# Performance work log

Hardware: AMD Instinct MI355X
Metric: run time of the kernel (lower is better)

Reference implementation:

```python
import jax, jax.numpy as jnp
import numpy as np

EPS = 1e-08
GUMBEL_TEMP = 1.0
TOPK = 5


def setup_inputs() -> dict:
    key = jax.random.key(0)
    k1, k2, k3, k4, k5, k6 = jax.random.split(key, 6)
    return {
        "h": jax.random.normal(k1, (64, 16), dtype=jnp.float32),
        "input": jax.random.normal(k2, (64, 16), dtype=jnp.float32),
        "w_p": jax.random.normal(k3, (16, 16), dtype=jnp.float32),
        "bias": jax.random.normal(k4, (64, 16), dtype=jnp.float32),
        "U1": jax.random.uniform(k5, (64, 4, 4), dtype=jnp.float32),
        "U2": jax.random.uniform(k6, (64, 4, 4), dtype=jnp.float32),
    }


def reference(h, input, w_p, bias, U1, U2):
    B = input.shape[0]  # 64 (hardcoded in the original module)
    h = h.reshape(B, 16)

    # Conditional range-remap when |h| exceeds 100 (data-dependent -> jnp.where)
    h_min, h_max = jnp.min(h), jnp.max(h)
    out_of_range = (h_max > 100.0) | (h_min < -100.0)
    mapped = jnp.clip((h - h_min) / (h_max - h_min) * 0.6 - 0.3, -0.3, 0.3)
    h = jnp.where(out_of_range, mapped, h)

    # small matmul + bias -> logits, reshaped to (64, 4, 4)
    mask = (h @ w_p + bias).reshape(64, 4, 4)

    # Gumbel noise difference
    g1 = -jnp.log(-jnp.log(U1 + EPS) + EPS)
    g2 = -jnp.log(-jnp.log(U2 + EPS) + EPS)
    soft = jax.nn.sigmoid((mask + g1 - g2) / GUMBEL_TEMP)

    # batched per-row top-k (k=5) over the flattened 4x4 grid
    flat = soft.reshape(64, 16)
    topv, _ = jax.lax.top_k(flat, TOPK)
    fifth = topv[:, TOPK - 1].reshape(64, 1, 1)

    # straight-through hard mask
    hard_bin = (soft >= fifth).astype(soft.dtype)
    hard = jax.lax.stop_gradient(hard_bin - soft) + soft
    return hard
```

## Files before the change

kernel.cpp:

```cpp
#include <hip/hip_runtime.h>
#include <math.h>

#define G_EPS 1e-8f

__global__ __launch_bounds__(1024) void GumbelLinear_kernel(
    const float* __restrict__ h_in,
    const float* __restrict__ w_p,
    const float* __restrict__ bias,
    const float* __restrict__ U1,
    const float* __restrict__ U2,
    float* __restrict__ out)
{
    __shared__ float h_s[64][16];
    __shared__ float w_s[16][16];
    __shared__ float s_s[64][16];
    __shared__ float wmin_s[16];
    __shared__ float wmax_s[16];
    __shared__ float gmm[2];

    const int tid = threadIdx.x;
    const int b   = tid >> 4;
    const int j   = tid & 15;

    float hv = h_in[tid];
    if (tid < 256) w_s[tid >> 4][tid & 15] = w_p[tid];

    float mn = hv, mx = hv;
    #pragma unroll
    for (int off = 32; off > 0; off >>= 1) {
        mn = fminf(mn, __shfl_down(mn, off));
        mx = fmaxf(mx, __shfl_down(mx, off));
    }
    const int lane = tid & 63;
    const int wid  = tid >> 6;
    if (lane == 0) { wmin_s[wid] = mn; wmax_s[wid] = mx; }
    __syncthreads();
    if (tid == 0) {
        float m0 = wmin_s[0], m1 = wmax_s[0];
        #pragma unroll
        for (int i = 1; i < 16; ++i) {
            m0 = fminf(m0, wmin_s[i]);
            m1 = fmaxf(m1, wmax_s[i]);
        }
        gmm[0] = m0; gmm[1] = m1;
    }
    __syncthreads();
    const float gmin = gmm[0], gmax = gmm[1];

    if (gmax > 100.0f || gmin < -100.0f) {
        float m = (hv - gmin) / (gmax - gmin) * 0.6f - 0.3f;
        hv = fminf(fmaxf(m, -0.3f), 0.3f);
    }
    h_s[b][j] = hv;
    __syncthreads();

    float acc = bias[tid];
    #pragma unroll
    for (int k = 0; k < 16; ++k) acc += h_s[b][k] * w_s[k][j];

    const float u1 = U1[tid], u2 = U2[tid];
    const float g1 = -logf(-logf(u1 + G_EPS) + G_EPS);
    const float g2 = -logf(-logf(u2 + G_EPS) + G_EPS);
    const float x  = acc + g1 - g2;
    const float soft = 1.0f / (1.0f + expf(-x));

    s_s[b][j] = soft;
    __syncthreads();

    int cnt = 0;
    #pragma unroll
    for (int k = 0; k < 16; ++k) cnt += (s_s[b][k] > soft) ? 1 : 0;

    const float hb = (cnt <= 4) ? 1.0f : 0.0f;
    out[tid] = (hb - soft) + soft;
}

extern "C" void kernel_launch(void* const* d_in, const int* in_sizes, int n_in,
                              void* d_out, int out_size, void* d_ws, size_t ws_size,
                              hipStream_t stream) {
    const float* h    = (const float*)d_in[0];
    const float* w_p  = (const float*)d_in[2];
    const float* bias = (const float*)d_in[3];
    const float* U1   = (const float*)d_in[4];
    const float* U2   = (const float*)d_in[5];
    float* out = (float*)d_out;

    GumbelLinear_kernel<<<1, 1024, 0, stream>>>(h, w_p, bias, U1, U2, out);
}
```

Measured before the change: 9.676 us.

## Restructure kernel to 256 threads with float4 work and shuffle-based row exchange

Each thread now handles four consecutive elements loaded as float4, so a 16-wide row spans four lanes. The row matmul and the top-k rank counting exchange values through xor shuffles instead of shared-memory staging, which removes two block barriers and the serial reduction step. The sigmoid is dropped and ranking is done on the pre-sigmoid logits, which is valid because sigmoid is monotonic. The output is written as exact 0/1 values rather than the (hb - soft) + soft straight-through form, which may differ from the reference in the last bit.

After: 16.31 us. 68.6% more time.

```diff
diff --git a/kernel.cpp b/kernel.cpp
--- a/kernel.cpp
+++ b/kernel.cpp
@@ -3,7 +3,7 @@
 
 #define G_EPS 1e-8f
 
-__global__ __launch_bounds__(1024) void GumbelLinear_kernel(
+__global__ __launch_bounds__(256) void GumbelLinear_kernel(
     const float* __restrict__ h_in,
     const float* __restrict__ w_p,
     const float* __restrict__ bias,
@@ -11,68 +11,89 @@
     const float* __restrict__ U2,
     float* __restrict__ out)
 {
-    __shared__ float h_s[64][16];
     __shared__ float w_s[16][16];
-    __shared__ float s_s[64][16];
-    __shared__ float wmin_s[16];
-    __shared__ float wmax_s[16];
-    __shared__ float gmm[2];
+    __shared__ float pmin[4], pmax[4];
 
-    const int tid = threadIdx.x;
-    const int b   = tid >> 4;
-    const int j   = tid & 15;
+    const int t = threadIdx.x;
+    const int q = t & 3;
 
-    float hv = h_in[tid];
-    if (tid < 256) w_s[tid >> 4][tid & 15] = w_p[tid];
+    const float4 h4  = reinterpret_cast<const float4*>(h_in)[t];
+    const float4 b4  = reinterpret_cast<const float4*>(bias)[t];
+    const float4 u14 = reinterpret_cast<const float4*>(U1)[t];
+    const float4 u24 = reinterpret_cast<const float4*>(U2)[t];
 
-    float mn = hv, mx = hv;
+    if (t < 64) {
+        reinterpret_cast<float4*>(&w_s[0][0])[t] =
+            reinterpret_cast<const float4*>(w_p)[t];
+    }
+
+    float mn = fminf(fminf(h4.x, h4.y), fminf(h4.z, h4.w));
+    float mx = fmaxf(fmaxf(h4.x, h4.y), fmaxf(h4.z, h4.w));
     #pragma unroll
-    for (int off = 32; off > 0; off >>= 1) {
-        mn = fminf(mn, __shfl_down(mn, off));
-        mx = fmaxf(mx, __shfl_down(mx, off));
+    for (int off = 1; off < 64; off <<= 1) {
+        mn = fminf(mn, __shfl_xor(mn, off));
+        mx = fmaxf(mx, __shfl_xor(mx, off));
     }
-    const int lane = tid & 63;
-    const int wid  = tid >> 6;
-    if (lane == 0) { wmin_s[wid] = mn; wmax_s[wid] = mx; }
+    if ((t & 63) == 0) { pmin[t >> 6] = mn; pmax[t >> 6] = mx; }
     __syncthreads();
-    if (tid == 0) {
-        float m0 = wmin_s[0], m1 = wmax_s[0];
-        #pragma unroll
-        for (int i = 1; i < 16; ++i) {
-            m0 = fminf(m0, wmin_s[i]);
-            m1 = fmaxf(m1, wmax_s[i]);
-        }
-        gmm[0] = m0; gmm[1] = m1;
+    const float gmin = fminf(fminf(pmin[0], pmin[1]), fminf(pmin[2], pmin[3]));
+    const float gmax = fmaxf(fmaxf(pmax[0], pmax[1]), fmaxf(pmax[2], pmax[3]));
+
+    float hx = h4.x, hy = h4.y, hz = h4.z, hw = h4.w;
+    if (gmax > 100.0f || gmin < -100.0f) {
+        const float r = gmax - gmin;
+        hx = fminf(fmaxf((hx - gmin) / r * 0.6f - 0.3f, -0.3f), 0.3f);
+        hy = fminf(fmaxf((hy - gmin) / r * 0.6f - 0.3f, -0.3f), 0.3f);
+        hz = fminf(fmaxf((hz - gmin) / r * 0.6f - 0.3f, -0.3f), 0.3f);
+        hw = fminf(fmaxf((hw - gmin) / r * 0.6f - 0.3f, -0.3f), 0.3f);
     }
-    __syncthreads();
-    const float gmin = gmm[0], gmax = gmm[1];
 
-    if (gmax > 100.0f || gmin < -100.0f) {
-        float m = (hv - gmin) / (gmax - gmin) * 0.6f - 0.3f;
-        hv = fminf(fmaxf(m, -0.3f), 0.3f);
+    float4 acc = b4;
+    const int jb = q << 2;
+    #pragma unroll
+    for (int m = 0; m < 4; ++m) {
+        const float v0 = __shfl_xor(hx, m);
+        const float v1 = __shfl_xor(hy, m);
+        const float v2 = __shfl_xor(hz, m);
+        const float v3 = __shfl_xor(hw, m);
+        const int kq = (q ^ m) << 2;
+        const float4 w0 = *reinterpret_cast<const float4*>(&w_s[kq + 0][jb]);
+        const float4 w1 = *reinterpret_cast<const float4*>(&w_s[kq + 1][jb]);
+        const float4 w2 = *reinterpret_cast<const float4*>(&w_s[kq + 2][jb]);
+        const float4 w3 = *reinterpret_cast<const float4*>(&w_s[kq + 3][jb]);
+        acc.x += v0 * w0.x + v1 * w1.x + v2 * w2.x + v3 * w3.x;
+        acc.y += v0 * w0.y + v1 * w1.y + v2 * w2.y + v3 * w3.y;
+        acc.z += v0 * w0.z + v1 * w1.z + v2 * w2.z + v3 * w3.z;
+        acc.w += v0 * w0.w + v1 * w1.w + v2 * w2.w + v3 * w3.w;
     }
-    h_s[b][j] = hv;
-    __syncthreads();
 
-    float acc = bias[tid];
+    const float xx = acc.x + logf(-logf(u24.x + G_EPS) + G_EPS) - logf(-logf(u14.x + G_EPS) + G_EPS);
+    const float xy = acc.y + logf(-logf(u24.y + G_EPS) + G_EPS) - logf(-logf(u14.y + G_EPS) + G_EPS);
+    const float xz = acc.z + logf(-logf(u24.z + G_EPS) + G_EPS) - logf(-logf(u14.z + G_EPS) + G_EPS);
+    const float xw = acc.w + logf(-logf(u24.w + G_EPS) + G_EPS) - logf(-logf(u14.w + G_EPS) + G_EPS);
+
+    int cx = (xy > xx) + (xz > xx) + (xw > xx);
+    int cy = (xx > xy) + (xz > xy) + (xw > xy);
+    int cz = (xx > xz) + (xy > xz) + (xw > xz);
+    int cw = (xx > xw) + (xy > xw) + (xz > xw);
     #pragma unroll
-    for (int k = 0; k < 16; ++k) acc += h_s[b][k] * w_s[k][j];
+    for (int m = 1; m < 4; ++m) {
+        const float v0 = __shfl_xor(xx, m);
+        const float v1 = __shfl_xor(xy, m);
+        const float v2 = __shfl_xor(xz, m);
+        const float v3 = __shfl_xor(xw, m);
+        cx += (v0 > xx) + (v1 > xx) + (v2 > xx) + (v3 > xx);
+        cy += (v0 > xy) + (v1 > xy) + (v2 > xy) + (v3 > xy);
+        cz += (v0 > xz) + (v1 > xz) + (v2 > xz) + (v3 > xz);
+        cw += (v0 > xw) + (v1 > xw) + (v2 > xw) + (v3 > xw);
+    }
 
-    const float u1 = U1[tid], u2 = U2[tid];
-    const float g1 = -logf(-logf(u1 + G_EPS) + G_EPS);
-    const float g2 = -logf(-logf(u2 + G_EPS) + G_EPS);
-    const float x  = acc + g1 - g2;
-    const float soft = 1.0f / (1.0f + expf(-x));
-
-    s_s[b][j] = soft;
-    __syncthreads();
-
-    int cnt = 0;
-    #pragma unroll
-    for (int k = 0; k < 16; ++k) cnt += (s_s[b][k] > soft) ? 1 : 0;
-
-    const float hb = (cnt <= 4) ? 1.0f : 0.0f;
-    out[tid] = (hb - soft) + soft;
+    float4 o;
+    o.x = (cx <= 4) ? 1.0f : 0.0f;
+    o.y = (cy <= 4) ? 1.0f : 0.0f;
+    o.z = (cz <= 4) ? 1.0f : 0.0f;
+    o.w = (cw <= 4) ? 1.0f : 0.0f;
+    reinterpret_cast<float4*>(out)[t] = o;
 }
 
 extern "C" void kernel_launch(void* const* d_in, const int* in_sizes, int n_in,
@@ -85,5 +106,5 @@
     const float* U2   = (const float*)d_in[5];
     float* out = (float*)d_out;
 
-    GumbelLinear_kernel<<<1, 1024, 0, stream>>>(h, w_p, bias, U1, U2, out);
+    GumbelLinear_kernel<<<1, 256, 0, stream>>>(h, w_p, bias, U1, U2, out);
 }
```
